# Performance work log

Hardware: AMD Instinct MI355X
Metric: run time of the kernel (lower is better)

Reference implementation:

```python
import jax, jax.numpy as jnp
import numpy as np

IN_CH, OUT_CH, KH, KW = 512, 512, 3, 3
LR_MULT = 1.0
WEIGHT_SCALE = LR_MULT / np.sqrt(IN_CH * KH * KW)


def setup_inputs() -> dict:
    key = jax.random.key(0)
    k1, k2, k3 = jax.random.split(key, 3)
    x = jax.random.normal(k1, (16, IN_CH, 32, 32), dtype=jnp.float32)
    s = jax.random.normal(k2, (16, IN_CH), dtype=jnp.float32)
    weight = jax.random.normal(k3, (OUT_CH, IN_CH, KH, KW), dtype=jnp.float32) / LR_MULT
    return {"x": x, "s": s, "weight": weight}


def reference(x, s, weight):
    B, Cin, H, Wd = x.shape
    Cout = weight.shape[0]
    W = weight * WEIGHT_SCALE                          # [Cout, Cin, kH, kW]
    # per-sample modulation: [B, Cout, Cin, kH, kW]
    Wm = s[:, None, :, None, None] * W[None]
    # demodulation: normalize each (b, out_channel) filter
    sigma = jnp.sqrt(jnp.sum(Wm ** 2, axis=(-3, -2, -1), keepdims=True) + 1e-8)
    Wm = Wm / sigma
    # grouped conv with groups = B
    x_g = x.reshape(1, B * Cin, H, Wd)
    W_g = Wm.reshape(B * Cout, Cin, KH, KW)
    out = jax.lax.conv_general_dilated(
        x_g, W_g,
        window_strides=(1, 1),
        padding="SAME",
        rhs_dilation=(1, 1),
        feature_group_count=B,
        dimension_numbers=("NCHW", "OIHW", "NCHW"),
    )
    return out.reshape(B, Cout, out.shape[-2], out.shape[-1])
```

## Files before the change

kernel.cpp:

```cpp
#include <hip/hip_runtime.h>
#include <hip/hip_bf16.h>


typedef __attribute__((ext_vector_type(4))) float f32x4;
typedef __attribute__((ext_vector_type(8))) short bf16x8;

#define NB    16
#define CIN   512
#define COUT  512
#define KTOT  4608
#define NPIX  (NB * 32 * 32)

#define WAITV0() asm volatile("s_waitcnt vmcnt(0)" ::: "memory")
#define FENCE()  asm volatile("" ::: "memory")
#define BAR()    { FENCE(); __builtin_amdgcn_s_barrier(); FENCE(); }

__device__ __forceinline__ void gload_lds16(const void* g, void* l) {
  __builtin_amdgcn_global_load_lds(
      (__attribute__((address_space(1))) void*)(g),
      (__attribute__((address_space(3))) void*)(l), 16, 0, 0);
}

__device__ __forceinline__ float bf16bits_to_f32(short v) {
  return __uint_as_float(((unsigned)(unsigned short)v) << 16);
}

__global__ __launch_bounds__(256) void pack_w_kernel(
    const float* __restrict__ w, __hip_bfloat16* __restrict__ wB3,
    float* __restrict__ wsq) {
  const int idx = blockIdx.x * 256 + threadIdx.x;
  const int o = idx >> 9, ci = idx & 511;
  const float* wp = w + (size_t)idx * 9;
  const float WSCALE = 0.014731391274719739f;
  float sum = 0.f;
#pragma unroll
  for (int t = 0; t < 9; ++t) {
    float v = wp[t] * WSCALE;
    sum += v * v;
    wB3[(size_t)o * KTOT + (((ci >> 6) * 9 + t) << 6) + (ci & 63)] =
        __float2bfloat16(v);
  }
  wsq[idx] = sum;
}

__global__ __launch_bounds__(256) void calc_rsig_kernel(
    const float* __restrict__ s, const float* __restrict__ wsq,
    float* __restrict__ rsig) {
  const int wid = blockIdx.x * 4 + (threadIdx.x >> 6);
  const int lane = threadIdx.x & 63;
  const int b = wid >> 9, o = wid & 511;
  const float* sp = s + b * 512;
  const float* wp = wsq + o * 512;
  float sum = 0.f;
#pragma unroll
  for (int i = 0; i < 8; ++i) {
    float sv = sp[lane + i * 64];
    sum += sv * sv * wp[lane + i * 64];
  }
#pragma unroll
  for (int off = 32; off > 0; off >>= 1) sum += __shfl_down(sum, off, 64);
  if (lane == 0) rsig[wid] = 1.0f / sqrtf(sum + 1e-8f);
}

__global__ __launch_bounds__(256) void modulate_kernel(
    const float* __restrict__ x, const float* __restrict__ s,
    __hip_bfloat16* __restrict__ xpad) {
  const int by = blockIdx.x;
  const int b = by >> 5, y = by & 31;
  __shared__ __attribute__((aligned(16))) __hip_bfloat16 tile[32][72];
  const int tid = threadIdx.x;
  const int xc = tid & 31;
  const int cr0 = tid >> 5;
  const float* xrow = x + ((size_t)b * 512 * 32 + y) * 32;
  const float* sb = s + b * 512;
  __hip_bfloat16* orow = xpad + (size_t)((b * 34 + y + 1) * 34) * 512;

  for (int ci0 = 0; ci0 < 512; ci0 += 64) {
#pragma unroll
    for (int r = 0; r < 8; ++r) {
      const int cir = r * 8 + cr0;
      const int ci = ci0 + cir;
      float v = xrow[(size_t)ci * 1024 + xc] * sb[ci];
      tile[xc][cir] = __float2bfloat16(v);
    }
    __syncthreads();
    const int xcw = tid >> 3, vec = tid & 7;
    bf16x8 v = *(const bf16x8*)&tile[xcw][vec * 8];
    *(bf16x8*)(orow + (size_t)(xcw + 1) * 512 + ci0 + vec * 8) = v;
    __syncthreads();
  }
}

__global__ __launch_bounds__(256) void halo_zero_kernel(
    __hip_bfloat16* __restrict__ xpad) {
  const int sb = blockIdx.x;
  const int b = sb / 132, s = sb - b * 132;
  int y, x;
  if (s < 34)       { y = 0;        x = s; }
  else if (s < 68)  { y = 33;       x = s - 34; }
  else if (s < 100) { y = s - 67;   x = 0; }
  else              { y = s - 99;   x = 33; }
  unsigned* p = (unsigned*)(xpad + (size_t)((b * 34 + y) * 34 + x) * 512);
  p[threadIdx.x] = 0u;
}

__global__ __launch_bounds__(256, 2) void conv_gemm_kernel(
    const __hip_bfloat16* __restrict__ wB3,
    const __hip_bfloat16* __restrict__ xpad,
    const float* __restrict__ rsig,
    float* __restrict__ out,
    __hip_bfloat16* __restrict__ p0,
    __hip_bfloat16* __restrict__ p1) {
  extern __shared__ __attribute__((aligned(16))) char ldsc[];

  const int tid = threadIdx.x;
  const int wv = tid >> 6, lane = tid & 63, l15 = lane & 15;
  const int bo0 = blockIdx.y << 7;
  const int bp0 = blockIdx.x << 8;
  const int z = blockIdx.z;
  const int bimg = blockIdx.x >> 2;
  const int y0 = (blockIdx.x & 3) << 3;
  const int wr = wv >> 1, wc = wv & 1;

  int gA[4];
#pragma unroll
  for (int r = 0; r < 4; ++r) {
    const int c = r * 256 + tid, row = c >> 3, sc = (c & 7) ^ (row & 7);
    gA[r] = (bo0 + row) * KTOT + sc * 8;
  }
  int gBs[11];
#pragma unroll
  for (int r = 0; r < 11; ++r) {
    const int u = r * 256 + tid;
    int R = u >> 3; if (R > 339) R = 339;
    const int c = u & 7, sc = c ^ (R & 7);
    const int yl = R / 34, xl = R - yl * 34;
    gBs[r] = ((bimg * 34 + y0 + yl) * 34 + xl) * 512 + sc * 8;
  }
  int Rb[8];
#pragma unroll
  for (int ni = 0; ni < 8; ++ni) {
    const int p = (wc << 7) + (ni << 4) + l15;
    Rb[ni] = (p >> 5) * 34 + (p & 31);
  }

  auto stageA = [&](int kt_next, int ktg_next) {
    char* dst = ldsc + (kt_next & 1) * 16384;
#pragma unroll
    for (int r = 0; r < 4; ++r)
      gload_lds16(wB3 + (size_t)(gA[r] + (ktg_next << 6)),
                  dst + (r * 256 + tid) * 16);
  };
  auto stageB = [&](int gg) {
    const int cio = ((z << 2) + gg) << 6;
    char* dst = ldsc + 32768;
#pragma unroll
    for (int r = 0; r < 11; ++r)
      gload_lds16(xpad + (size_t)(gBs[r] + cio), dst + (r * 256 + tid) * 16);
  };

  f32x4 acc[4][8];
#pragma unroll
  for (int mi = 0; mi < 4; ++mi)
#pragma unroll
    for (int ni = 0; ni < 8; ++ni) acc[mi][ni] = f32x4{0.f, 0.f, 0.f, 0.f};

  const int kb0 = (lane >> 4) << 4;

  stageB(0);
  stageA(0, z * 36);
  WAITV0();
  BAR();

#pragma unroll 1
  for (int g = 0; g < 4; ++g) {
#pragma unroll 1
    for (int tap = 0; tap < 9; ++tap) {
      const int kt = g * 9 + tap;
      if (kt < 35) stageA(kt + 1, z * 36 + kt + 1);
      const char* bufA = ldsc + (kt & 1) * 16384;
      const char* bufB = ldsc + 32768;
      const int ty = (tap * 11) >> 5;
      const int tapoff = tap + 31 * ty;

      bf16x8 af[4][2];
#pragma unroll
      for (int mi = 0; mi < 4; ++mi) {
        const int row = (wr << 6) + (mi << 4) + l15;
        const int swz = (row & 7) << 4;
        af[mi][0] = *(const bf16x8*)(bufA + row * 128 + (kb0 ^ swz));
        af[mi][1] = *(const bf16x8*)(bufA + row * 128 + ((64 | kb0) ^ swz));
      }
      {
        bf16x8 bv[8];
#pragma unroll
        for (int ni = 0; ni < 8; ++ni) {
          const int R = Rb[ni] + tapoff;
          bv[ni] = *(const bf16x8*)(bufB + R * 128 + (kb0 ^ ((R & 7) << 4)));
        }
        __builtin_amdgcn_s_setprio(1);
#pragma unroll
        for (int mi = 0; mi < 4; ++mi)
#pragma unroll
          for (int ni = 0; ni < 8; ++ni)
            acc[mi][ni] = __builtin_amdgcn_mfma_f32_16x16x32_bf16(
                af[mi][0], bv[ni], acc[mi][ni], 0, 0, 0);
        __builtin_amdgcn_s_setprio(0);
      }
      {
        bf16x8 bv[8];
#pragma unroll
        for (int ni = 0; ni < 8; ++ni) {
          const int R = Rb[ni] + tapoff;
          bv[ni] = *(const bf16x8*)(bufB + R * 128 +
                                    ((64 | kb0) ^ ((R & 7) << 4)));
        }
        if (tap == 8 && g < 3) { BAR(); stageB(g + 1); }
        __builtin_amdgcn_s_setprio(1);
#pragma unroll
        for (int mi = 0; mi < 4; ++mi)
#pragma unroll
          for (int ni = 0; ni < 8; ++ni)
            acc[mi][ni] = __builtin_amdgcn_mfma_f32_16x16x32_bf16(
                af[mi][1], bv[ni], acc[mi][ni], 0, 0, 0);
        __builtin_amdgcn_s_setprio(0);
      }
      WAITV0();
      BAR();
    }
  }

  __hip_bfloat16* pz = z ? p1 : p0;
  const bool f32path = (p0 == nullptr) && (z == 0);
#pragma unroll
  for (int mi = 0; mi < 4; ++mi) {
    const int o = bo0 + (wr << 6) + (mi << 4) + ((lane >> 4) << 2);
    const f32x4 rs = *(const f32x4*)(rsig + (bimg << 9) + o);
#pragma unroll
    for (int ni = 0; ni < 8; ++ni) {
      const int p = bp0 + (wc << 7) + (ni << 4) + l15;
      const int prem = p & 1023;
#pragma unroll
      for (int r = 0; r < 4; ++r) {
        const float v = acc[mi][ni][r] * rs[r];
        const size_t oidx = ((size_t)((bimg << 9) + o + r)) * 1024 + prem;
        if (f32path) out[oidx] = v;
        else pz[oidx] = __float2bfloat16(v);
      }
    }
  }
}

__global__ __launch_bounds__(256) void merge2_kernel(
    float* __restrict__ out, const __hip_bfloat16* __restrict__ p0,
    const __hip_bfloat16* __restrict__ p1) {
  const size_t i = (size_t)blockIdx.x * 256 + threadIdx.x;
  const bf16x8 a = ((const bf16x8*)p0)[i];
  const bf16x8 b = ((const bf16x8*)p1)[i];
  f32x4 o0, o1;
#pragma unroll
  for (int j = 0; j < 4; ++j) {
    o0[j] = bf16bits_to_f32(a[j]) + bf16bits_to_f32(b[j]);
    o1[j] = bf16bits_to_f32(a[4 + j]) + bf16bits_to_f32(b[4 + j]);
  }
  ((f32x4*)out)[2 * i] = o0;
  ((f32x4*)out)[2 * i + 1] = o1;
}

__global__ __launch_bounds__(256) void merge1_kernel(
    float* __restrict__ out, const __hip_bfloat16* __restrict__ p1) {
  const size_t i = (size_t)blockIdx.x * 256 + threadIdx.x;
  f32x4* o4 = (f32x4*)out + 2 * i;
  f32x4 a = o4[0], b = o4[1];
  const bf16x8 pv = ((const bf16x8*)p1)[i];
#pragma unroll
  for (int j = 0; j < 4; ++j) {
    a[j] += bf16bits_to_f32(pv[j]);
    b[j] += bf16bits_to_f32(pv[4 + j]);
  }
  o4[0] = a;
  o4[1] = b;
}

extern "C" void kernel_launch(void* const* d_in, const int* in_sizes, int n_in,
                              void* d_out, int out_size, void* d_ws,
                              size_t ws_size, hipStream_t stream) {
  const float* x = (const float*)d_in[0];
  const float* s = (const float*)d_in[1];
  const float* w = (const float*)d_in[2];
  float* out = (float*)d_out;

  char* ws = (char*)d_ws;
  const size_t xpad_bytes = (size_t)NB * 34 * 34 * 512 * 2;
  const size_t wB_bytes = (size_t)COUT * KTOT * 2;
  const size_t wsq_bytes = (size_t)COUT * CIN * 4;
  const size_t rsig_bytes = (size_t)NB * COUT * 4;
  const size_t part_bytes = (size_t)NPIX * COUT * 2;
  __hip_bfloat16* xpad = (__hip_bfloat16*)ws;
  __hip_bfloat16* wB3 = (__hip_bfloat16*)(ws + xpad_bytes);
  float* wsq = (float*)(ws + xpad_bytes + wB_bytes);
  float* rsig = (float*)(ws + xpad_bytes + wB_bytes + wsq_bytes);
  char* pbase = ws + xpad_bytes + wB_bytes + wsq_bytes + rsig_bytes;
  __hip_bfloat16* p1 = (__hip_bfloat16*)pbase;
  __hip_bfloat16* p0 = (__hip_bfloat16*)(pbase + part_bytes);
  const bool two_partials =
      ws_size >= (xpad_bytes + wB_bytes + wsq_bytes + rsig_bytes +
                  2 * part_bytes);

  const int lds_bytes = 77824;
  hipFuncSetAttribute((const void*)conv_gemm_kernel,
                      hipFuncAttributeMaxDynamicSharedMemorySize, lds_bytes);

  halo_zero_kernel<<<NB * 132, 256, 0, stream>>>(xpad);
  pack_w_kernel<<<(COUT * CIN) / 256, 256, 0, stream>>>(w, wB3, wsq);
  modulate_kernel<<<NB * 32, 256, 0, stream>>>(x, s, xpad);
  calc_rsig_kernel<<<(NB * COUT) / 4, 256, 0, stream>>>(s, wsq, rsig);
  conv_gemm_kernel<<<dim3(NPIX / 256, COUT / 128, 2), 256, lds_bytes, stream>>>(
      wB3, xpad, rsig, out, two_partials ? p0 : nullptr, p1);
  const int mblocks = (NPIX * COUT / 8) / 256;
  if (two_partials)
    merge2_kernel<<<mblocks, 256, 0, stream>>>(out, p0, p1);
  else
    merge1_kernel<<<mblocks, 256, 0, stream>>>(out, p1);
}
```

Baseline: 102.4 us.

## Restructure conv GEMM into 256x256 tiles with 8-wave double-buffered ping-pong schedule

The implicit-GEMM conv kernel moves from 128x256 tiles with 4 waves to 256x256 tiles with 8 waves (512 threads). Both A and B are double-buffered in 128 KB of LDS. The main loop is split into barrier-separated quadrants of MFMAs, with global-to-LDS loads for the next K-step interleaved and partial vmcnt waits. B is now reloaded per tap directly from the padded input instead of staging a halo tile once and reusing it across the 9 taps. This raises arithmetic intensity and overlaps loads with MFMA, but it issues more global B traffic, adds many barriers, and allows only one block per CU because of the LDS footprint.

```diff
diff --git a/kernel.cpp b/kernel.cpp
--- a/kernel.cpp
+++ b/kernel.cpp
@@ -11,7 +11,11 @@
 #define KTOT  4608
 #define NPIX  (NB * 32 * 32)
 
+#define WAITV8() asm volatile("s_waitcnt vmcnt(8)" ::: "memory")
+#define WAITV6() asm volatile("s_waitcnt vmcnt(6)" ::: "memory")
 #define WAITV0() asm volatile("s_waitcnt vmcnt(0)" ::: "memory")
+#define LGKM0()  asm volatile("s_waitcnt lgkmcnt(0)" ::: "memory")
+#define SB0()    __builtin_amdgcn_sched_barrier(0)
 #define FENCE()  asm volatile("" ::: "memory")
 #define BAR()    { FENCE(); __builtin_amdgcn_s_barrier(); FENCE(); }
 
@@ -104,7 +108,17 @@
   p[threadIdx.x] = 0u;
 }
 
-__global__ __launch_bounds__(256, 2) void conv_gemm_kernel(
+#define QUAD(MI0, NI0)                                                        \
+  _Pragma("unroll")                                                           \
+  for (int mi = (MI0); mi < (MI0) + 2; ++mi)                                  \
+    _Pragma("unroll")                                                         \
+    for (int ni = (NI0); ni < (NI0) + 4; ++ni)                                \
+      _Pragma("unroll")                                                       \
+      for (int kk = 0; kk < 2; ++kk)                                          \
+        acc[mi][ni] = __builtin_amdgcn_mfma_f32_16x16x32_bf16(                \
+            af[mi][kk], bv[ni][kk], acc[mi][ni], 0, 0, 0);
+
+__global__ __launch_bounds__(512, 2) void conv_gemm_kernel(
     const __hip_bfloat16* __restrict__ wB3,
     const __hip_bfloat16* __restrict__ xpad,
     const float* __restrict__ rsig,
@@ -115,48 +129,54 @@
 
   const int tid = threadIdx.x;
   const int wv = tid >> 6, lane = tid & 63, l15 = lane & 15;
-  const int bo0 = blockIdx.y << 7;
+  const int k16 = ((lane >> 4) & 3) << 4;
+  const int bo0 = blockIdx.y << 8;
   const int bp0 = blockIdx.x << 8;
   const int z = blockIdx.z;
   const int bimg = blockIdx.x >> 2;
-  const int y0 = (blockIdx.x & 3) << 3;
   const int wr = wv >> 1, wc = wv & 1;
 
-  int gA[4];
-#pragma unroll
-  for (int r = 0; r < 4; ++r) {
-    const int c = r * 256 + tid, row = c >> 3, sc = (c & 7) ^ (row & 7);
-    gA[r] = (bo0 + row) * KTOT + sc * 8;
-  }
-  int gBs[11];
-#pragma unroll
-  for (int r = 0; r < 11; ++r) {
-    const int u = r * 256 + tid;
-    int R = u >> 3; if (R > 339) R = 339;
-    const int c = u & 7, sc = c ^ (R & 7);
-    const int yl = R / 34, xl = R - yl * 34;
-    gBs[r] = ((bimg * 34 + y0 + yl) * 34 + xl) * 512 + sc * 8;
-  }
-  int Rb[8];
-#pragma unroll
-  for (int ni = 0; ni < 8; ++ni) {
-    const int p = (wc << 7) + (ni << 4) + l15;
-    Rb[ni] = (p >> 5) * 34 + (p & 31);
-  }
-
-  auto stageA = [&](int kt_next, int ktg_next) {
-    char* dst = ldsc + (kt_next & 1) * 16384;
-#pragma unroll
-    for (int r = 0; r < 4; ++r)
-      gload_lds16(wB3 + (size_t)(gA[r] + (ktg_next << 6)),
-                  dst + (r * 256 + tid) * 16);
-  };
-  auto stageB = [&](int gg) {
-    const int cio = ((z << 2) + gg) << 6;
-    char* dst = ldsc + 32768;
-#pragma unroll
-    for (int r = 0; r < 11; ++r)
-      gload_lds16(xpad + (size_t)(gBs[r] + cio), dst + (r * 256 + tid) * 16);
+  int aoff[2];
+#pragma unroll
+  for (int rr = 0; rr < 2; ++rr) {
+    const int c = rr * 512 + tid, row = c >> 3, sc = (c & 7) ^ (row & 7);
+    aoff[rr] = (bo0 + row) * KTOT + sc * 8;
+  }
+  int boff[2][2];
+#pragma unroll
+  for (int rr = 0; rr < 2; ++rr)
+#pragma unroll
+    for (int h = 0; h < 2; ++h) {
+      const int c = rr * 512 + tid, row = c >> 3, sc = (c & 7) ^ (row & 7);
+      const int p = bp0 + h * 128 + row, b = p >> 10, rem = p & 1023,
+                y = rem >> 5, xx = rem & 31;
+      boff[rr][h] = ((b * 34 + y) * 34 + xx) * 512 + sc * 8;
+    }
+
+  auto stA = [&](int par, int ktg, int h) {
+    char* dst = ldsc + par * 65536 + h * 16384 + tid * 16;
+    gload_lds16(wB3 + (size_t)(aoff[0] + h * (128 * KTOT) + (ktg << 6)), dst);
+    gload_lds16(wB3 + (size_t)(aoff[1] + h * (128 * KTOT) + (ktg << 6)),
+                dst + 8192);
+  };
+  auto stB = [&](int par, int h, int xo) {
+    char* dst = ldsc + par * 65536 + 32768 + h * 16384 + tid * 16;
+    gload_lds16(xpad + (size_t)(boff[0][h] + xo), dst);
+    gload_lds16(xpad + (size_t)(boff[1][h] + xo), dst + 8192);
+  };
+  auto xoff_of = [&](int ktg) {
+    const int g = ktg / 9, tp = ktg - 9 * g;
+    return (tp + 31 * (tp / 3)) * 512 + (g << 6);
+  };
+  auto rdA = [&](const char* buf, int mi, int kk) -> bf16x8 {
+    const int row = (wr << 6) + (mi << 4) + l15;
+    return *(const bf16x8*)(buf + row * 128 +
+                            (((kk << 6) | k16) ^ ((row & 7) << 4)));
+  };
+  auto rdB = [&](const char* buf, int ni, int kk) -> bf16x8 {
+    const int row = (wc << 7) + (ni << 4) + l15;
+    return *(const bf16x8*)(buf + row * 128 +
+                            (((kk << 6) | k16) ^ ((row & 7) << 4)));
   };
 
   f32x4 acc[4][8];
@@ -165,69 +185,116 @@
 #pragma unroll
     for (int ni = 0; ni < 8; ++ni) acc[mi][ni] = f32x4{0.f, 0.f, 0.f, 0.f};
 
-  const int kb0 = (lane >> 4) << 4;
-
-  stageB(0);
-  stageA(0, z * 36);
-  WAITV0();
-  BAR();
+  {
+    const int g0 = z * 36;
+    const int x0 = xoff_of(g0), x1 = xoff_of(g0 + 1);
+    stA(0, g0, 0); stA(0, g0, 1); stB(0, 0, x0); stB(0, 1, x0);
+    stA(1, g0 + 1, 0); stA(1, g0 + 1, 1); stB(1, 0, x1); stB(1, 1, x1);
+    WAITV0();
+    BAR();
+  }
+
+  const char* A0 = ldsc;
+  const char* B0 = ldsc + 32768;
+  const char* A1 = ldsc + 65536;
+  const char* B1 = ldsc + 98304;
 
 #pragma unroll 1
-  for (int g = 0; g < 4; ++g) {
-#pragma unroll 1
-    for (int tap = 0; tap < 9; ++tap) {
-      const int kt = g * 9 + tap;
-      if (kt < 35) stageA(kt + 1, z * 36 + kt + 1);
-      const char* bufA = ldsc + (kt & 1) * 16384;
-      const char* bufB = ldsc + 32768;
-      const int ty = (tap * 11) >> 5;
-      const int tapoff = tap + 31 * ty;
-
-      bf16x8 af[4][2];
-#pragma unroll
-      for (int mi = 0; mi < 4; ++mi) {
-        const int row = (wr << 6) + (mi << 4) + l15;
-        const int swz = (row & 7) << 4;
-        af[mi][0] = *(const bf16x8*)(bufA + row * 128 + (kb0 ^ swz));
-        af[mi][1] = *(const bf16x8*)(bufA + row * 128 + ((64 | kb0) ^ swz));
-      }
-      {
-        bf16x8 bv[8];
-#pragma unroll
-        for (int ni = 0; ni < 8; ++ni) {
-          const int R = Rb[ni] + tapoff;
-          bv[ni] = *(const bf16x8*)(bufB + R * 128 + (kb0 ^ ((R & 7) << 4)));
-        }
-        __builtin_amdgcn_s_setprio(1);
-#pragma unroll
-        for (int mi = 0; mi < 4; ++mi)
-#pragma unroll
-          for (int ni = 0; ni < 8; ++ni)
-            acc[mi][ni] = __builtin_amdgcn_mfma_f32_16x16x32_bf16(
-                af[mi][0], bv[ni], acc[mi][ni], 0, 0, 0);
-        __builtin_amdgcn_s_setprio(0);
-      }
-      {
-        bf16x8 bv[8];
-#pragma unroll
-        for (int ni = 0; ni < 8; ++ni) {
-          const int R = Rb[ni] + tapoff;
-          bv[ni] = *(const bf16x8*)(bufB + R * 128 +
-                                    ((64 | kb0) ^ ((R & 7) << 4)));
-        }
-        if (tap == 8 && g < 3) { BAR(); stageB(g + 1); }
-        __builtin_amdgcn_s_setprio(1);
-#pragma unroll
-        for (int mi = 0; mi < 4; ++mi)
-#pragma unroll
-          for (int ni = 0; ni < 8; ++ni)
-            acc[mi][ni] = __builtin_amdgcn_mfma_f32_16x16x32_bf16(
-                af[mi][1], bv[ni], acc[mi][ni], 0, 0, 0);
-        __builtin_amdgcn_s_setprio(0);
-      }
-      WAITV0();
-      BAR();
-    }
+  for (int t = 0; t < 18; ++t) {
+    const int ktg0 = z * 36 + 2 * t;
+    const bool s2 = (2 * t + 2) < 36, s3 = (2 * t + 3) < 36;
+    int x2 = 0, x3 = 0;
+    if (s2) x2 = xoff_of(ktg0 + 2);
+    if (s3) x3 = xoff_of(ktg0 + 3);
+
+    bf16x8 af[4][2], bv[8][2];
+
+#pragma unroll
+    for (int mi = 0; mi < 2; ++mi) {
+      af[mi][0] = rdA(A0, mi, 0); af[mi][1] = rdA(A0, mi, 1);
+    }
+#pragma unroll
+    for (int ni = 0; ni < 4; ++ni) {
+      bv[ni][0] = rdB(B0, ni, 0); bv[ni][1] = rdB(B0, ni, 1);
+    }
+    BAR(); LGKM0(); SB0();
+    __builtin_amdgcn_s_setprio(1);
+    QUAD(0, 0);
+    __builtin_amdgcn_s_setprio(0);
+    BAR();
+
+#pragma unroll
+    for (int mi = 2; mi < 4; ++mi) {
+      af[mi][0] = rdA(A0, mi, 0); af[mi][1] = rdA(A0, mi, 1);
+    }
+    BAR(); LGKM0(); SB0();
+    __builtin_amdgcn_s_setprio(1);
+    QUAD(2, 0);
+    __builtin_amdgcn_s_setprio(0);
+    BAR();
+
+#pragma unroll
+    for (int ni = 4; ni < 8; ++ni) {
+      bv[ni][0] = rdB(B0, ni, 0); bv[ni][1] = rdB(B0, ni, 1);
+    }
+    if (s2) stA(0, ktg0 + 2, 0);
+    BAR(); LGKM0(); SB0();
+    __builtin_amdgcn_s_setprio(1);
+    QUAD(2, 4);
+    __builtin_amdgcn_s_setprio(0);
+    BAR();
+
+    if (s2) { stA(0, ktg0 + 2, 1); stB(0, 0, x2); }
+    BAR();
+    __builtin_amdgcn_s_setprio(1);
+    QUAD(0, 4);
+    __builtin_amdgcn_s_setprio(0);
+    if (t < 17) { WAITV6(); } else { WAITV0(); }
+    BAR();
+
+#pragma unroll
+    for (int mi = 0; mi < 2; ++mi) {
+      af[mi][0] = rdA(A1, mi, 0); af[mi][1] = rdA(A1, mi, 1);
+    }
+#pragma unroll
+    for (int ni = 0; ni < 4; ++ni) {
+      bv[ni][0] = rdB(B1, ni, 0); bv[ni][1] = rdB(B1, ni, 1);
+    }
+    if (s2) stB(0, 1, x2);
+    BAR(); LGKM0(); SB0();
+    __builtin_amdgcn_s_setprio(1);
+    QUAD(0, 0);
+    __builtin_amdgcn_s_setprio(0);
+    BAR();
+
+#pragma unroll
+    for (int mi = 2; mi < 4; ++mi) {
+      af[mi][0] = rdA(A1, mi, 0); af[mi][1] = rdA(A1, mi, 1);
+    }
+    BAR(); LGKM0(); SB0();
+    __builtin_amdgcn_s_setprio(1);
+    QUAD(2, 0);
+    __builtin_amdgcn_s_setprio(0);
+    BAR();
+
+#pragma unroll
+    for (int ni = 4; ni < 8; ++ni) {
+      bv[ni][0] = rdB(B1, ni, 0); bv[ni][1] = rdB(B1, ni, 1);
+    }
+    if (s3) stA(1, ktg0 + 3, 0);
+    BAR(); LGKM0(); SB0();
+    __builtin_amdgcn_s_setprio(1);
+    QUAD(2, 4);
+    __builtin_amdgcn_s_setprio(0);
+    BAR();
+
+    if (s3) { stA(1, ktg0 + 3, 1); stB(1, 0, x3); stB(1, 1, x3); }
+    BAR();
+    __builtin_amdgcn_s_setprio(1);
+    QUAD(0, 4);
+    __builtin_amdgcn_s_setprio(0);
+    if (t < 17) { WAITV8(); }
+    BAR();
   }
 
   __hip_bfloat16* pz = z ? p1 : p0;
@@ -307,7 +374,7 @@
       ws_size >= (xpad_bytes + wB_bytes + wsq_bytes + rsig_bytes +
                   2 * part_bytes);
 
-  const int lds_bytes = 77824;
+  const int lds_bytes = 131072;
   hipFuncSetAttribute((const void*)conv_gemm_kernel,
                       hipFuncAttributeMaxDynamicSharedMemorySize, lds_bytes);
 
@@ -315,8 +382,9 @@
   pack_w_kernel<<<(COUT * CIN) / 256, 256, 0, stream>>>(w, wB3, wsq);
   modulate_kernel<<<NB * 32, 256, 0, stream>>>(x, s, xpad);
   calc_rsig_kernel<<<(NB * COUT) / 4, 256, 0, stream>>>(s, wsq, rsig);
-  conv_gemm_kernel<<<dim3(NPIX / 256, COUT / 128, 2), 256, lds_bytes, stream>>>(
-      wB3, xpad, rsig, out, two_partials ? p0 : nullptr, p1);
+  conv_gemm_kernel<<<dim3(NPIX / 256, COUT / 256, 2), 512, lds_bytes,
+                     stream>>>(wB3, xpad, rsig, out,
+                               two_partials ? p0 : nullptr, p1);
   const int mblocks = (NPIX * COUT / 8) / 256;
   if (two_partials)
     merge2_kernel<<<mblocks, 256, 0, stream>>>(out, p0, p1);
```

New measurement: 107.4 us. 1.05x slower.
